# Optimization experiments

Hardware: AMD Instinct MI355X
Metric: run time of the kernel (lower is better)

The kernel has to match this reference:

```python
import jax, jax.numpy as jnp
import numpy as np

B, T, D, R = 4, 2048, 1024, 32


def setup_inputs() -> dict:
    key = jax.random.key(0)
    kx, ku = jax.random.split(key)
    x = jax.random.normal(kx, (B, T, D), dtype=jnp.float32)
    # low-rank metric factor; small init so distances are moderate
    U = jax.random.normal(ku, (D, R), dtype=jnp.float32) * 0.05
    return {"x": x, "U": U}


def reference(x, U):
    # g = U @ U.T (PSD low-rank metric).
    # dist_sq[b,t,j] = (x_t - x_j)^T g (x_t - x_j)
    #               = ||U^T x_t||^2 + ||U^T x_j||^2 - 2 (U^T x_t).(U^T x_j)
    # Algebraic expansion of the original O(B*T*T*D) broadcasted diff tensor.
    y = jnp.einsum('btd,dr->btr', x, U)                # [B,T,R]
    n = jnp.sum(y * y, axis=-1)                         # [B,T]
    cross = jnp.einsum('btr,bjr->btj', y, y)            # [B,T,T]
    dist_sq = n[:, :, None] + n[:, None, :] - 2.0 * cross
    attn = jax.nn.softmax(-dist_sq, axis=-1)            # [B,T,T]
    return jnp.einsum('btj,bjd->btd', attn, x)          # [B,T,D]
```

## Files before the change

### kernel.cpp

```cpp
#include <hip/hip_runtime.h>

#define B_ 4
#define T_ 2048
#define D_ 1024
#define R_ 32
#define XSTR2 136

typedef __attribute__((ext_vector_type(8))) short short8;
typedef __attribute__((ext_vector_type(4))) float f32x4;
typedef __attribute__((ext_vector_type(4))) unsigned short us4;
typedef __attribute__((ext_vector_type(8))) unsigned short us8;

__device__ __forceinline__ unsigned short f2bf(float f) {
  union { float f; unsigned u; } v; v.f = f;
  unsigned r = (v.u + 0x7fffu + ((v.u >> 16) & 1u)) >> 16;
  return (unsigned short)r;
}
__device__ __forceinline__ float bf2f(unsigned short h) {
  union { unsigned u; float f; } v; v.u = (unsigned)h << 16;
  return v.f;
}

__global__ __launch_bounds__(256)
void geo_ut(const float* __restrict__ U, unsigned short* __restrict__ Ut) {
  __shared__ float tile[128][33];
  const int tid = threadIdx.x;
  const int d0 = blockIdx.x * 128;
  #pragma unroll
  for (int i = 0; i < 16; i++) {
    int e = i * 256 + tid;
    int d = e >> 5, r = e & 31;
    tile[d][r] = U[(size_t)(d0 + d) * R_ + r];
  }
  __syncthreads();
  const int r = tid >> 3, seg = tid & 7;
  us8 o0, o1;
  #pragma unroll
  for (int k = 0; k < 8; k++) o0[k] = f2bf(tile[seg * 16 + k][r]);
  #pragma unroll
  for (int k = 0; k < 8; k++) o1[k] = f2bf(tile[seg * 16 + 8 + k][r]);
  *(us8*)(Ut + (size_t)r * D_ + d0 + seg * 16) = o0;
  *(us8*)(Ut + (size_t)r * D_ + d0 + seg * 16 + 8) = o1;
}

__global__ __launch_bounds__(256)
void geo_prep(const float* __restrict__ x, const unsigned short* __restrict__ Ut,
              unsigned short* __restrict__ xt, float* __restrict__ y_part) {
  __shared__ unsigned short xs[2][32 * XSTR2];
  const int b = blockIdx.y, slab = blockIdx.z;
  const int t0 = blockIdx.x * 32;
  const int d0 = slab * 256;
  const int tid = threadIdx.x, w = tid >> 6, lane = tid & 63;
  const int m = lane & 15, quad = lane >> 4;
  const int Mt = w & 1, Nt = w >> 1;
  const int lr = tid >> 3;
  const int lc = (tid & 7) * 16;

  const float* xb = x + ((size_t)b * T_ + t0 + lr) * D_ + d0 + lc;
  float4 v[2][4];
  #pragma unroll
  for (int ch = 0; ch < 2; ch++)
    #pragma unroll
    for (int i = 0; i < 4; i++)
      v[ch][i] = *(const float4*)(xb + ch * 128 + i * 4);
  #pragma unroll
  for (int ch = 0; ch < 2; ch++)
    #pragma unroll
    for (int i = 0; i < 4; i++) {
      us4 c;
      c[0] = f2bf(v[ch][i].x); c[1] = f2bf(v[ch][i].y);
      c[2] = f2bf(v[ch][i].z); c[3] = f2bf(v[ch][i].w);
      *(us4*)&xs[ch][lr * XSTR2 + lc + i * 4] = c;
    }
  __syncthreads();
  {
    const int wd = tid >> 1, wt = (tid & 1) * 16;
    #pragma unroll
    for (int ch = 0; ch < 2; ch++) {
      us8 o0, o1;
      #pragma unroll
      for (int k = 0; k < 8; k++) {
        o0[k] = xs[ch][(wt + k) * XSTR2 + wd];
        o1[k] = xs[ch][(wt + 8 + k) * XSTR2 + wd];
      }
      unsigned short* xo = xt + ((size_t)b * D_ + d0 + ch * 128 + wd) * T_ + t0;
      *(us8*)(xo + wt) = o0;
      *(us8*)(xo + wt + 8) = o1;
    }
  }
  f32x4 acc = {0.f, 0.f, 0.f, 0.f};
  #pragma unroll
  for (int ch = 0; ch < 2; ch++)
    #pragma unroll
    for (int ks = 0; ks < 4; ks++) {
      short8 af = *(const short8*)&xs[ch][(Mt * 16 + m) * XSTR2 + ks * 32 + quad * 8];
      short8 bf = *(const short8*)(Ut + (size_t)(Nt * 16 + m) * D_ + d0 + ch * 128 + ks * 32 + quad * 8);
      acc = __builtin_amdgcn_mfma_f32_16x16x32_bf16(af, bf, acc, 0, 0, 0);
    }
  float* yp = y_part + ((size_t)(slab * B_ + b) * T_ + t0 + Mt * 16 + quad * 4) * R_ + Nt * 16 + m;
  #pragma unroll
  for (int k = 0; k < 4; k++) yp[(size_t)k * R_] = acc[k];
}

__global__ __launch_bounds__(256)
void geo_reduce(const float* __restrict__ y_part, unsigned short* __restrict__ ybf,
                float* __restrict__ nsq) {
  const int tid = threadIdx.x;
  const size_t row = (size_t)blockIdx.x * 32 + (tid >> 3);
  const int r0 = (tid & 7) * 4;
  f32x4 v = {0.f, 0.f, 0.f, 0.f};
  #pragma unroll
  for (int s = 0; s < 4; s++) {
    f32x4 p = *(const f32x4*)(y_part + ((size_t)s * B_ * T_ + row) * R_ + r0);
    #pragma unroll
    for (int k = 0; k < 4; k++) v[k] += p[k];
  }
  us4 pk;
  float part = 0.f;
  #pragma unroll
  for (int k = 0; k < 4; k++) {
    pk[k] = f2bf(1.69864446f * v[k]);
    float b = bf2f(pk[k]);
    part += b * b;
  }
  *(us4*)(ybf + row * R_ + r0) = pk;
  part += __shfl_xor(part, 1, 64);
  part += __shfl_xor(part, 2, 64);
  part += __shfl_xor(part, 4, 64);
  if ((tid & 7) == 0) nsq[row] = 0.5f * part;
}

__global__ __launch_bounds__(256, 2)
void geo_fused(const unsigned short* __restrict__ ybf,
               const float* __restrict__ nsq,
               const unsigned short* __restrict__ xt,
               float* __restrict__ out) {
  __shared__ unsigned short As[128 * 64];
  __shared__ unsigned short Bs[128 * 64];
  __shared__ float l_s[128];
  const int b = blockIdx.z;
  const int id = blockIdx.x;
  const int d0 = (id & 7) * 128;
  const int t0 = (id >> 3) * 128;
  const int tid = threadIdx.x, w = tid >> 6, lane = tid & 63;
  const int m = lane & 15, quad = lane >> 4;
  const int wr = (w & 1) * 64, wc = (w >> 1) * 64;
  const int srow = lane >> 3, sslot = lane & 7;
  const int tw = w * 32;

  const unsigned short* yb = ybf + (size_t)b * T_ * R_;
  const float* nb = nsq + b * T_;
  const unsigned short* Xb = xt + ((size_t)b * D_ + d0) * T_;

  short8 at[2]; float nnt[2]; float lsum[2] = {0.f, 0.f};
  #pragma unroll
  for (int tb = 0; tb < 2; tb++) {
    at[tb] = *(const short8*)(yb + (size_t)(t0 + tw + tb * 16 + m) * R_ + quad * 8);
    nnt[tb] = -nb[t0 + tw + tb * 16 + m];
  }

  f32x4 acc[4][4];
  #pragma unroll
  for (int i = 0; i < 4; i++)
    #pragma unroll
    for (int j = 0; j < 4; j++) acc[i][j] = (f32x4){0.f, 0.f, 0.f, 0.f};

  short8 aj[4]; f32x4 njv[4];
  #pragma unroll
  for (int ja = 0; ja < 4; ja++) {
    aj[ja] = *(const short8*)(yb + (size_t)(ja * 16 + m) * R_ + quad * 8);
    njv[ja] = *(const f32x4*)(nb + ja * 16 + quad * 4);
  }

  for (int j0 = 0; j0 < T_; j0 += 64) {
    __syncthreads();
    #pragma unroll
    for (int cc = 0; cc < 4; cc++) {
      const int row = w * 32 + cc * 8 + srow;
      const int gs = sslot ^ (row & 7);
      __builtin_amdgcn_global_load_lds(
          (const __attribute__((address_space(1))) void*)(Xb + (size_t)row * T_ + j0 + gs * 8),
          (__attribute__((address_space(3))) void*)(Bs + (w * 32 + cc * 8) * 64),
          16, 0, 0);
    }
    short8 caj[4]; f32x4 cnj[4];
    #pragma unroll
    for (int ja = 0; ja < 4; ja++) { caj[ja] = aj[ja]; cnj[ja] = njv[ja]; }
    const int jn = (j0 + 64 < T_) ? j0 + 64 : 0;
    #pragma unroll
    for (int ja = 0; ja < 4; ja++) {
      aj[ja] = *(const short8*)(yb + (size_t)(jn + ja * 16 + m) * R_ + quad * 8);
      njv[ja] = *(const f32x4*)(nb + jn + ja * 16 + quad * 4);
    }
    #pragma unroll
    for (int tb = 0; tb < 2; tb++) {
      const int trow = tw + tb * 16 + m;
      #pragma unroll
      for (int ja = 0; ja < 4; ja++) {
        f32x4 cin;
        #pragma unroll
        for (int r = 0; r < 4; r++) cin[r] = nnt[tb] - cnj[ja][r];
        f32x4 c = __builtin_amdgcn_mfma_f32_16x16x32_bf16(caj[ja], at[tb], cin, 0, 0, 0);
        us4 pk; float ls = 0.f;
        #pragma unroll
        for (int r = 0; r < 4; r++) {
          float p = __builtin_amdgcn_exp2f(c[r]);
          ls += p;
          pk[r] = f2bf(p);
        }
        lsum[tb] += ls;
        const int sb = ja * 2 + (quad >> 1);
        char* dst = (char*)As + trow * 128 + ((sb ^ (trow & 7)) * 16) + (quad & 1) * 8;
        *(us4*)dst = pk;
      }
    }
    __syncthreads();
    #pragma unroll
    for (int ks = 0; ks < 2; ks++) {
      short8 af[4], bf[4];
      #pragma unroll
      for (int i = 0; i < 4; i++) {
        const int ra = wr + i * 16 + m;
        af[i] = *(const short8*)(As + ra * 64 + (((ks * 4 + quad) ^ (m & 7)) * 8));
        const int cd = wc + i * 16 + m;
        bf[i] = *(const short8*)(Bs + cd * 64 + (((ks * 4 + quad) ^ (m & 7)) * 8));
      }
      #pragma unroll
      for (int rb = 0; rb < 4; rb++)
        #pragma unroll
        for (int cb = 0; cb < 4; cb++)
          acc[rb][cb] = __builtin_amdgcn_mfma_f32_16x16x32_bf16(af[rb], bf[cb], acc[rb][cb], 0, 0, 0);
    }
  }
  #pragma unroll
  for (int tb = 0; tb < 2; tb++) {
    lsum[tb] += __shfl_xor(lsum[tb], 16, 64);
    lsum[tb] += __shfl_xor(lsum[tb], 32, 64);
  }
  if (quad == 0) { l_s[tw + m] = lsum[0]; l_s[tw + 16 + m] = lsum[1]; }
  __syncthreads();
  float* ob = out + ((size_t)b * T_ + t0 + wr) * D_ + d0 + wc;
  #pragma unroll
  for (int rb = 0; rb < 4; rb++) {
    f32x4 lv = *(const f32x4*)&l_s[wr + rb * 16 + quad * 4];
    f32x4 inv;
    #pragma unroll
    for (int r = 0; r < 4; r++) inv[r] = 1.f / lv[r];
    #pragma unroll
    for (int cb = 0; cb < 4; cb++)
      #pragma unroll
      for (int r = 0; r < 4; r++)
        ob[(size_t)(rb * 16 + quad * 4 + r) * D_ + cb * 16 + m] = acc[rb][cb][r] * inv[r];
  }
}

extern "C" void kernel_launch(void* const* d_in, const int* in_sizes, int n_in,
                              void* d_out, int out_size, void* d_ws, size_t ws_size,
                              hipStream_t stream) {
  const float* x = (const float*)d_in[0];
  const float* U = (const float*)d_in[1];
  float* out = (float*)d_out;

  const size_t xt_b  = (size_t)B_ * D_ * T_ * 2;
  const size_t ybf_b = (size_t)B_ * T_ * R_ * 2;
  const size_t nsq_b = (size_t)B_ * T_ * 4;
  const size_t ut_b  = (size_t)D_ * R_ * 2;
  const size_t yp_b  = (size_t)4 * B_ * T_ * R_ * 4;

  char* wp = (char*)d_ws;
  unsigned short* xtp = (unsigned short*)wp;                 wp += xt_b;
  unsigned short* ybf = (unsigned short*)wp;                 wp += ybf_b;
  float* nsq = (float*)wp;                                   wp += nsq_b;
  unsigned short* Utp = (unsigned short*)wp;                 wp += ut_b;
  float* ypart = (float*)wp;                                 wp += yp_b;
  (void)ws_size; (void)in_sizes; (void)n_in; (void)out_size;

  hipLaunchKernelGGL(geo_ut, dim3(D_ / 128), dim3(256), 0, stream, U, Utp);
  hipLaunchKernelGGL(geo_prep, dim3(T_ / 32, B_, 4), dim3(256), 0, stream,
                     x, Utp, xtp, ypart);
  hipLaunchKernelGGL(geo_reduce, dim3(B_ * T_ / 32), dim3(256), 0, stream,
                     ypart, ybf, nsq);
  hipLaunchKernelGGL(geo_fused, dim3((T_ / 128) * (D_ / 128), 1, B_), dim3(256), 0, stream,
                     ybf, nsq, xtp, out);
}
```

Before: 155.3 us.

## Keep softmax probabilities in registers and restructure prep/reduce kernels

The fused attention kernel no longer writes exp probabilities to shared memory. Each wave computes a 32-row by 128-column score tile whose MFMA output layout is permuted so it can feed the PV MFMA directly as the A operand, and the key tile grows to 128 columns with only the X tile in LDS. The U transpose kernel is folded into the prep kernel, which now handles 128x128 tiles with U staged in LDS and writes y partials transposed across 8 slabs, and the reduce kernel transposes through LDS. The aim is to remove LDS traffic, barriers and a launch, at the cost of more registers per thread and larger partial buffers.

```diff
diff --git a/kernel.cpp b/kernel.cpp
--- a/kernel.cpp
+++ b/kernel.cpp
@@ -4,7 +4,7 @@
 #define T_ 2048
 #define D_ 1024
 #define R_ 32
-#define XSTR2 136
+#define XP 136
 
 typedef __attribute__((ext_vector_type(8))) short short8;
 typedef __attribute__((ext_vector_type(4))) float f32x4;
@@ -22,112 +22,119 @@
 }
 
 __global__ __launch_bounds__(256)
-void geo_ut(const float* __restrict__ U, unsigned short* __restrict__ Ut) {
-  __shared__ float tile[128][33];
-  const int tid = threadIdx.x;
-  const int d0 = blockIdx.x * 128;
-  #pragma unroll
-  for (int i = 0; i < 16; i++) {
-    int e = i * 256 + tid;
-    int d = e >> 5, r = e & 31;
-    tile[d][r] = U[(size_t)(d0 + d) * R_ + r];
-  }
-  __syncthreads();
-  const int r = tid >> 3, seg = tid & 7;
-  us8 o0, o1;
-  #pragma unroll
-  for (int k = 0; k < 8; k++) o0[k] = f2bf(tile[seg * 16 + k][r]);
-  #pragma unroll
-  for (int k = 0; k < 8; k++) o1[k] = f2bf(tile[seg * 16 + 8 + k][r]);
-  *(us8*)(Ut + (size_t)r * D_ + d0 + seg * 16) = o0;
-  *(us8*)(Ut + (size_t)r * D_ + d0 + seg * 16 + 8) = o1;
-}
-
-__global__ __launch_bounds__(256)
-void geo_prep(const float* __restrict__ x, const unsigned short* __restrict__ Ut,
-              unsigned short* __restrict__ xt, float* __restrict__ y_part) {
-  __shared__ unsigned short xs[2][32 * XSTR2];
-  const int b = blockIdx.y, slab = blockIdx.z;
-  const int t0 = blockIdx.x * 32;
-  const int d0 = slab * 256;
+void geo_prep(const float* __restrict__ x, const float* __restrict__ U,
+              unsigned short* __restrict__ xt, float* __restrict__ ypart) {
+  __shared__ unsigned short xs[128 * XP];
+  __shared__ unsigned short uts[32 * XP];
+  const int bb = blockIdx.y, t0 = blockIdx.x * 128, d0 = blockIdx.z * 128;
   const int tid = threadIdx.x, w = tid >> 6, lane = tid & 63;
   const int m = lane & 15, quad = lane >> 4;
-  const int Mt = w & 1, Nt = w >> 1;
-  const int lr = tid >> 3;
-  const int lc = (tid & 7) * 16;
-
-  const float* xb = x + ((size_t)b * T_ + t0 + lr) * D_ + d0 + lc;
-  float4 v[2][4];
-  #pragma unroll
-  for (int ch = 0; ch < 2; ch++)
-    #pragma unroll
-    for (int i = 0; i < 4; i++)
-      v[ch][i] = *(const float4*)(xb + ch * 128 + i * 4);
-  #pragma unroll
-  for (int ch = 0; ch < 2; ch++)
-    #pragma unroll
-    for (int i = 0; i < 4; i++) {
-      us4 c;
-      c[0] = f2bf(v[ch][i].x); c[1] = f2bf(v[ch][i].y);
-      c[2] = f2bf(v[ch][i].z); c[3] = f2bf(v[ch][i].w);
-      *(us4*)&xs[ch][lr * XSTR2 + lc + i * 4] = c;
-    }
+
+  f32x4 uv[4];
+  #pragma unroll
+  for (int p = 0; p < 4; p++) {
+    const int i4 = p * 256 + tid;
+    uv[p] = *(const f32x4*)(U + (size_t)(d0 + (i4 >> 3)) * R_ + (i4 & 7) * 4);
+  }
+  f32x4 xv[16];
+  #pragma unroll
+  for (int p = 0; p < 16; p++) {
+    const int i4 = p * 256 + tid;
+    xv[p] = *(const f32x4*)(x + ((size_t)bb * T_ + t0 + (i4 >> 5)) * D_ + d0 + (i4 & 31) * 4);
+  }
+  #pragma unroll
+  for (int p = 0; p < 4; p++) {
+    const int i4 = p * 256 + tid; const int du = i4 >> 3, ru4 = i4 & 7;
+    #pragma unroll
+    for (int k = 0; k < 4; k++) uts[(ru4 * 4 + k) * XP + du] = f2bf(uv[p][k]);
+  }
+  #pragma unroll
+  for (int p = 0; p < 16; p++) {
+    const int i4 = p * 256 + tid; const int r = i4 >> 5, c4 = i4 & 31;
+    us4 c;
+    c[0] = f2bf(xv[p][0]); c[1] = f2bf(xv[p][1]);
+    c[2] = f2bf(xv[p][2]); c[3] = f2bf(xv[p][3]);
+    *(us4*)&xs[r * XP + c4 * 4] = c;
+  }
   __syncthreads();
   {
-    const int wd = tid >> 1, wt = (tid & 1) * 16;
-    #pragma unroll
-    for (int ch = 0; ch < 2; ch++) {
-      us8 o0, o1;
-      #pragma unroll
-      for (int k = 0; k < 8; k++) {
-        o0[k] = xs[ch][(wt + k) * XSTR2 + wd];
-        o1[k] = xs[ch][(wt + 8 + k) * XSTR2 + wd];
-      }
-      unsigned short* xo = xt + ((size_t)b * D_ + d0 + ch * 128 + wd) * T_ + t0;
-      *(us8*)(xo + wt) = o0;
-      *(us8*)(xo + wt + 8) = o1;
-    }
-  }
-  f32x4 acc = {0.f, 0.f, 0.f, 0.f};
-  #pragma unroll
-  for (int ch = 0; ch < 2; ch++)
-    #pragma unroll
-    for (int ks = 0; ks < 4; ks++) {
-      short8 af = *(const short8*)&xs[ch][(Mt * 16 + m) * XSTR2 + ks * 32 + quad * 8];
-      short8 bf = *(const short8*)(Ut + (size_t)(Nt * 16 + m) * D_ + d0 + ch * 128 + ks * 32 + quad * 8);
-      acc = __builtin_amdgcn_mfma_f32_16x16x32_bf16(af, bf, acc, 0, 0, 0);
-    }
-  float* yp = y_part + ((size_t)(slab * B_ + b) * T_ + t0 + Mt * 16 + quad * 4) * R_ + Nt * 16 + m;
-  #pragma unroll
-  for (int k = 0; k < 4; k++) yp[(size_t)k * R_] = acc[k];
+    const int d = tid >> 1, th = tid & 1;
+    unsigned short* xo = xt + ((size_t)bb * D_ + d0 + d) * T_ + t0 + th * 64;
+    #pragma unroll
+    for (int i = 0; i < 8; i++) {
+      us8 o;
+      #pragma unroll
+      for (int k = 0; k < 8; k++) o[k] = xs[(th * 64 + i * 8 + k) * XP + d];
+      *(us8*)(xo + i * 8) = o;
+    }
+  }
+  f32x4 acc[2][2];
+  #pragma unroll
+  for (int i = 0; i < 2; i++)
+    #pragma unroll
+    for (int j = 0; j < 2; j++) acc[i][j] = (f32x4){0.f, 0.f, 0.f, 0.f};
+  #pragma unroll
+  for (int ks = 0; ks < 4; ks++) {
+    const int ko = ks * 32 + quad * 8;
+    short8 a0 = *(const short8*)&xs[(w * 32 + m) * XP + ko];
+    short8 a1 = *(const short8*)&xs[(w * 32 + 16 + m) * XP + ko];
+    short8 b0 = *(const short8*)&uts[m * XP + ko];
+    short8 b1 = *(const short8*)&uts[(16 + m) * XP + ko];
+    acc[0][0] = __builtin_amdgcn_mfma_f32_16x16x32_bf16(a0, b0, acc[0][0], 0, 0, 0);
+    acc[0][1] = __builtin_amdgcn_mfma_f32_16x16x32_bf16(a0, b1, acc[0][1], 0, 0, 0);
+    acc[1][0] = __builtin_amdgcn_mfma_f32_16x16x32_bf16(a1, b0, acc[1][0], 0, 0, 0);
+    acc[1][1] = __builtin_amdgcn_mfma_f32_16x16x32_bf16(a1, b1, acc[1][1], 0, 0, 0);
+  }
+  #pragma unroll
+  for (int tb = 0; tb < 2; tb++)
+    #pragma unroll
+    for (int nb = 0; nb < 2; nb++)
+      *(f32x4*)(ypart + ((size_t)(blockIdx.z * B_ + bb) * R_ + nb * 16 + m) * T_
+                + t0 + w * 32 + tb * 16 + quad * 4) = acc[tb][nb];
 }
 
 __global__ __launch_bounds__(256)
-void geo_reduce(const float* __restrict__ y_part, unsigned short* __restrict__ ybf,
+void geo_reduce(const float* __restrict__ ypart, unsigned short* __restrict__ ybf,
                 float* __restrict__ nsq) {
+  __shared__ float ls[32 * 132];
+  const int t0 = blockIdx.x * 128, bb = blockIdx.y;
   const int tid = threadIdx.x;
-  const size_t row = (size_t)blockIdx.x * 32 + (tid >> 3);
-  const int r0 = (tid & 7) * 4;
-  f32x4 v = {0.f, 0.f, 0.f, 0.f};
-  #pragma unroll
-  for (int s = 0; s < 4; s++) {
-    f32x4 p = *(const f32x4*)(y_part + ((size_t)s * B_ * T_ + row) * R_ + r0);
-    #pragma unroll
-    for (int k = 0; k < 4; k++) v[k] += p[k];
-  }
-  us4 pk;
-  float part = 0.f;
-  #pragma unroll
-  for (int k = 0; k < 4; k++) {
-    pk[k] = f2bf(1.69864446f * v[k]);
-    float b = bf2f(pk[k]);
-    part += b * b;
-  }
-  *(us4*)(ybf + row * R_ + r0) = pk;
+  f32x4 vs[4];
+  #pragma unroll
+  for (int p = 0; p < 4; p++) vs[p] = (f32x4){0.f, 0.f, 0.f, 0.f};
+  for (int s = 0; s < 8; s++) {
+    #pragma unroll
+    for (int p = 0; p < 4; p++) {
+      const int i4 = p * 256 + tid;
+      f32x4 v = *(const f32x4*)(ypart + ((size_t)(s * B_ + bb) * R_ + (i4 >> 5)) * T_
+                                + t0 + (i4 & 31) * 4);
+      #pragma unroll
+      for (int k = 0; k < 4; k++) vs[p][k] += v[k];
+    }
+  }
+  #pragma unroll
+  for (int p = 0; p < 4; p++) {
+    const int i4 = p * 256 + tid;
+    *(f32x4*)&ls[(i4 >> 5) * 132 + (i4 & 31) * 4] = vs[p];
+  }
+  __syncthreads();
+  const int t = tid >> 1, rh = tid & 1;
+  us8 o0, o1; float part = 0.f;
+  #pragma unroll
+  for (int k = 0; k < 8; k++) {
+    const unsigned short h = f2bf(1.69864446f * ls[(rh * 16 + k) * 132 + t]);
+    const float bv = bf2f(h); part += bv * bv; o0[k] = h;
+  }
+  #pragma unroll
+  for (int k = 0; k < 8; k++) {
+    const unsigned short h = f2bf(1.69864446f * ls[(rh * 16 + 8 + k) * 132 + t]);
+    const float bv = bf2f(h); part += bv * bv; o1[k] = h;
+  }
   part += __shfl_xor(part, 1, 64);
-  part += __shfl_xor(part, 2, 64);
-  part += __shfl_xor(part, 4, 64);
-  if ((tid & 7) == 0) nsq[row] = 0.5f * part;
+  unsigned short* yo = ybf + ((size_t)bb * T_ + t0 + t) * R_ + rh * 16;
+  *(us8*)yo = o0;
+  *(us8*)(yo + 8) = o1;
+  if (rh == 0) nsq[bb * T_ + t0 + t] = 0.5f * part;
 }
 
 __global__ __launch_bounds__(256, 2)
@@ -135,101 +142,83 @@
                const float* __restrict__ nsq,
                const unsigned short* __restrict__ xt,
                float* __restrict__ out) {
-  __shared__ unsigned short As[128 * 64];
-  __shared__ unsigned short Bs[128 * 64];
+  __shared__ unsigned short Bs[128 * 128];
   __shared__ float l_s[128];
-  const int b = blockIdx.z;
-  const int id = blockIdx.x;
+  const int bz = blockIdx.z, id = blockIdx.x;
   const int d0 = (id & 7) * 128;
   const int t0 = (id >> 3) * 128;
   const int tid = threadIdx.x, w = tid >> 6, lane = tid & 63;
   const int m = lane & 15, quad = lane >> 4;
-  const int wr = (w & 1) * 64, wc = (w >> 1) * 64;
-  const int srow = lane >> 3, sslot = lane & 7;
-  const int tw = w * 32;
-
-  const unsigned short* yb = ybf + (size_t)b * T_ * R_;
-  const float* nb = nsq + b * T_;
-  const unsigned short* Xb = xt + ((size_t)b * D_ + d0) * T_;
+  const int srow4 = lane >> 4, blk = lane & 15;
+
+  const unsigned short* yb = ybf + (size_t)bz * T_ * R_;
+  const float* nq = nsq + bz * T_;
+  const unsigned short* Xb = xt + ((size_t)bz * D_ + d0) * T_;
+
+#define STAGE(J0) do {                                                           \
+    _Pragma("unroll")                                                            \
+    for (int cc = 0; cc < 8; cc++) {                                             \
+      const int rbase = w * 32 + cc * 4;                                         \
+      const int row = rbase + srow4;                                             \
+      const int sw = (blk ^ (row & 7)) * 8;                                      \
+      __builtin_amdgcn_global_load_lds(                                          \
+        (const __attribute__((address_space(1))) void*)(Xb + (size_t)row * T_ + (J0) + sw), \
+        (__attribute__((address_space(3))) void*)(Bs + rbase * 128), 16, 0, 0);  \
+    } } while (0)
 
   short8 at[2]; float nnt[2]; float lsum[2] = {0.f, 0.f};
   #pragma unroll
   for (int tb = 0; tb < 2; tb++) {
-    at[tb] = *(const short8*)(yb + (size_t)(t0 + tw + tb * 16 + m) * R_ + quad * 8);
-    nnt[tb] = -nb[t0 + tw + tb * 16 + m];
-  }
-
-  f32x4 acc[4][4];
-  #pragma unroll
-  for (int i = 0; i < 4; i++)
-    #pragma unroll
-    for (int j = 0; j < 4; j++) acc[i][j] = (f32x4){0.f, 0.f, 0.f, 0.f};
-
-  short8 aj[4]; f32x4 njv[4];
-  #pragma unroll
-  for (int ja = 0; ja < 4; ja++) {
-    aj[ja] = *(const short8*)(yb + (size_t)(ja * 16 + m) * R_ + quad * 8);
-    njv[ja] = *(const f32x4*)(nb + ja * 16 + quad * 4);
-  }
-
-  for (int j0 = 0; j0 < T_; j0 += 64) {
+    at[tb] = *(const short8*)(yb + (size_t)(t0 + w * 32 + tb * 16 + m) * R_ + quad * 8);
+    nnt[tb] = -nq[t0 + w * 32 + tb * 16 + m];
+  }
+
+  f32x4 acc[2][8];
+  #pragma unroll
+  for (int i = 0; i < 2; i++)
+    #pragma unroll
+    for (int j = 0; j < 8; j++) acc[i][j] = (f32x4){0.f, 0.f, 0.f, 0.f};
+
+  for (int it = 0; it < 16; ++it) {
+    const int j0 = it * 128;
     __syncthreads();
-    #pragma unroll
-    for (int cc = 0; cc < 4; cc++) {
-      const int row = w * 32 + cc * 8 + srow;
-      const int gs = sslot ^ (row & 7);
-      __builtin_amdgcn_global_load_lds(
-          (const __attribute__((address_space(1))) void*)(Xb + (size_t)row * T_ + j0 + gs * 8),
-          (__attribute__((address_space(3))) void*)(Bs + (w * 32 + cc * 8) * 64),
-          16, 0, 0);
-    }
-    short8 caj[4]; f32x4 cnj[4];
-    #pragma unroll
-    for (int ja = 0; ja < 4; ja++) { caj[ja] = aj[ja]; cnj[ja] = njv[ja]; }
-    const int jn = (j0 + 64 < T_) ? j0 + 64 : 0;
-    #pragma unroll
-    for (int ja = 0; ja < 4; ja++) {
-      aj[ja] = *(const short8*)(yb + (size_t)(jn + ja * 16 + m) * R_ + quad * 8);
-      njv[ja] = *(const f32x4*)(nb + jn + ja * 16 + quad * 4);
-    }
+    STAGE(j0);
+    short8 aj[8]; f32x4 njv[8];
+    #pragma unroll
+    for (int ja = 0; ja < 8; ja++) {
+      const int jr = 32 * (ja >> 1) + 8 * (m >> 2) + (ja & 1) * 4 + (m & 3);
+      aj[ja] = *(const short8*)(yb + (size_t)(j0 + jr) * R_ + quad * 8);
+      njv[ja] = *(const f32x4*)(nq + j0 + 32 * (ja >> 1) + (ja & 1) * 4 + 8 * quad);
+    }
+    short8 pfrag[2][4];
     #pragma unroll
     for (int tb = 0; tb < 2; tb++) {
-      const int trow = tw + tb * 16 + m;
-      #pragma unroll
-      for (int ja = 0; ja < 4; ja++) {
+      #pragma unroll
+      for (int ja = 0; ja < 8; ja++) {
         f32x4 cin;
         #pragma unroll
-        for (int r = 0; r < 4; r++) cin[r] = nnt[tb] - cnj[ja][r];
-        f32x4 c = __builtin_amdgcn_mfma_f32_16x16x32_bf16(caj[ja], at[tb], cin, 0, 0, 0);
-        us4 pk; float ls = 0.f;
+        for (int r = 0; r < 4; r++) cin[r] = nnt[tb] - njv[ja][r];
+        f32x4 c = __builtin_amdgcn_mfma_f32_16x16x32_bf16(aj[ja], at[tb], cin, 0, 0, 0);
         #pragma unroll
         for (int r = 0; r < 4; r++) {
-          float p = __builtin_amdgcn_exp2f(c[r]);
-          ls += p;
-          pk[r] = f2bf(p);
+          const float p = __builtin_amdgcn_exp2f(c[r]);
+          lsum[tb] += p;
+          pfrag[tb][ja >> 1][(ja & 1) * 4 + r] = (short)f2bf(p);
         }
-        lsum[tb] += ls;
-        const int sb = ja * 2 + (quad >> 1);
-        char* dst = (char*)As + trow * 128 + ((sb ^ (trow & 7)) * 16) + (quad & 1) * 8;
-        *(us4*)dst = pk;
       }
     }
     __syncthreads();
     #pragma unroll
-    for (int ks = 0; ks < 2; ks++) {
-      short8 af[4], bf[4];
-      #pragma unroll
-      for (int i = 0; i < 4; i++) {
-        const int ra = wr + i * 16 + m;
-        af[i] = *(const short8*)(As + ra * 64 + (((ks * 4 + quad) ^ (m & 7)) * 8));
-        const int cd = wc + i * 16 + m;
-        bf[i] = *(const short8*)(Bs + cd * 64 + (((ks * 4 + quad) ^ (m & 7)) * 8));
-      }
-      #pragma unroll
-      for (int rb = 0; rb < 4; rb++)
+    for (int kb = 0; kb < 4; kb++) {
+      short8 bfr[8];
+      #pragma unroll
+      for (int nb = 0; nb < 8; nb++)
+        bfr[nb] = *(const short8*)&Bs[(nb * 16 + m) * 128 + (((kb * 4 + quad) ^ (m & 7)) * 8)];
+      #pragma unroll
+      for (int tb = 0; tb < 2; tb++)
         #pragma unroll
-        for (int cb = 0; cb < 4; cb++)
-          acc[rb][cb] = __builtin_amdgcn_mfma_f32_16x16x32_bf16(af[rb], bf[cb], acc[rb][cb], 0, 0, 0);
+        for (int nb = 0; nb < 8; nb++)
+          acc[tb][nb] = __builtin_amdgcn_mfma_f32_16x16x32_bf16(pfrag[tb][kb], bfr[nb], acc[tb][nb], 0, 0, 0);
     }
   }
   #pragma unroll
@@ -237,21 +226,22 @@
     lsum[tb] += __shfl_xor(lsum[tb], 16, 64);
     lsum[tb] += __shfl_xor(lsum[tb], 32, 64);
   }
-  if (quad == 0) { l_s[tw + m] = lsum[0]; l_s[tw + 16 + m] = lsum[1]; }
+  if (quad == 0) { l_s[w * 32 + m] = lsum[0]; l_s[w * 32 + 16 + m] = lsum[1]; }
   __syncthreads();
-  float* ob = out + ((size_t)b * T_ + t0 + wr) * D_ + d0 + wc;
-  #pragma unroll
-  for (int rb = 0; rb < 4; rb++) {
-    f32x4 lv = *(const f32x4*)&l_s[wr + rb * 16 + quad * 4];
+  #pragma unroll
+  for (int tb = 0; tb < 2; tb++) {
+    f32x4 lv = *(const f32x4*)&l_s[w * 32 + tb * 16 + quad * 4];
     f32x4 inv;
     #pragma unroll
     for (int r = 0; r < 4; r++) inv[r] = 1.f / lv[r];
-    #pragma unroll
-    for (int cb = 0; cb < 4; cb++)
+    float* ob = out + ((size_t)bz * T_ + t0 + w * 32 + tb * 16 + quad * 4) * D_ + d0;
+    #pragma unroll
+    for (int nb = 0; nb < 8; nb++)
       #pragma unroll
       for (int r = 0; r < 4; r++)
-        ob[(size_t)(rb * 16 + quad * 4 + r) * D_ + cb * 16 + m] = acc[rb][cb][r] * inv[r];
-  }
+        ob[(size_t)r * D_ + nb * 16 + m] = acc[tb][nb][r] * inv[r];
+  }
+#undef STAGE
 }
 
 extern "C" void kernel_launch(void* const* d_in, const int* in_sizes, int n_in,
@@ -264,21 +254,18 @@
   const size_t xt_b  = (size_t)B_ * D_ * T_ * 2;
   const size_t ybf_b = (size_t)B_ * T_ * R_ * 2;
   const size_t nsq_b = (size_t)B_ * T_ * 4;
-  const size_t ut_b  = (size_t)D_ * R_ * 2;
-  const size_t yp_b  = (size_t)4 * B_ * T_ * R_ * 4;
+  const size_t yp_b  = (size_t)8 * B_ * R_ * T_ * 4;
 
   char* wp = (char*)d_ws;
   unsigned short* xtp = (unsigned short*)wp;                 wp += xt_b;
   unsigned short* ybf = (unsigned short*)wp;                 wp += ybf_b;
   float* nsq = (float*)wp;                                   wp += nsq_b;
-  unsigned short* Utp = (unsigned short*)wp;                 wp += ut_b;
   float* ypart = (float*)wp;                                 wp += yp_b;
   (void)ws_size; (void)in_sizes; (void)n_in; (void)out_size;
 
-  hipLaunchKernelGGL(geo_ut, dim3(D_ / 128), dim3(256), 0, stream, U, Utp);
-  hipLaunchKernelGGL(geo_prep, dim3(T_ / 32, B_, 4), dim3(256), 0, stream,
-                     x, Utp, xtp, ypart);
-  hipLaunchKernelGGL(geo_reduce, dim3(B_ * T_ / 32), dim3(256), 0, stream,
+  hipLaunchKernelGGL(geo_prep, dim3(T_ / 128, B_, D_ / 128), dim3(256), 0, stream,
+                     x, U, xtp, ypart);
+  hipLaunchKernelGGL(geo_reduce, dim3(T_ / 128, B_), dim3(256), 0, stream,
                      ypart, ybf, nsq);
   hipLaunchKernelGGL(geo_fused, dim3((T_ / 128) * (D_ / 128), 1, B_), dim3(256), 0, stream,
                      ybf, nsq, xtp, out);
```

Result: slower. 176.3 us (+13.5%).
